# Kernel tuning notes

Hardware: AMD Instinct MI355X
Metric: run time of the kernel (lower is better)

The kernel has to match this reference:

```python
import jax, jax.numpy as jnp
import numpy as np

IMG_H, IMG_W = 240, 320
NEAR, FAR = 0.1, 10.0
CHUNK = 64  # triangles rasterized per scan step
CAM_K = np.array([[286.2057, 0.0, 162.6306],
                  [0.0, 286.7852, 121.0245],
                  [0.0, 0.0, 1.0]], np.float32)


def build_projection(cam, w, h, x0=0, y0=0, nc=NEAR, fc=FAR):
    q = -(fc + nc) / float(fc - nc)
    qn = -2.0 * fc * nc / float(fc - nc)
    proj = np.array([
        [2 * cam[0, 0] / w, -2 * cam[0, 1] / w, (-2 * cam[0, 2] + w + 2 * x0) / w, 0],
        [0, -2 * cam[1, 1] / h, (-2 * cam[1, 2] + h + 2 * y0) / h, 0],
        [0, 0, q, qn],
        [0, 0, -1, 0]], dtype=np.float64)
    proj[1, :] *= -1.0
    return jnp.asarray(proj.T, jnp.float32)


def vertex_normals(verts, faces):
    # per-face normal scattered to its vertices then renormalized
    # (equals dirt lighting.vertex_normals_pre_split on split meshes)
    v0, v1, v2 = verts[faces[:, 0]], verts[faces[:, 1]], verts[faces[:, 2]]
    fn = jnp.cross(v1 - v0, v2 - v0)
    fn = fn / jnp.maximum(jnp.linalg.norm(fn, axis=1, keepdims=True), 1e-12)
    vn = (jnp.zeros_like(verts)
          .at[faces[:, 0]].add(fn)
          .at[faces[:, 1]].add(fn)
          .at[faces[:, 2]].add(fn))
    return vn / jnp.maximum(jnp.linalg.norm(vn, axis=1, keepdims=True), 1e-12)


def transform_vertices(vertices, pose, faces, proj):
    vert_obj = jnp.concatenate([vertices, jnp.ones_like(vertices[:, -1:])], axis=1)  # [V,4]
    normals = vertex_normals(vert_obj[:, :3], faces)
    gl = jnp.array([[1., 0., 0.], [0., -1., 0.], [0., 0., -1.]], jnp.float32)
    rot = gl @ pose[:3, :3]
    # replicate the flat-list surgery: cam_pose[:3,:3]=gl@R, negate t_y, t_z
    cam_pose = pose.at[:3, :3].set(rot).at[1, 3].multiply(-1.0).at[2, 3].multiply(-1.0)
    view = cam_pose.T
    vert_cam = vert_obj @ view                                   # [V,4]
    vert_3d = vert_obj[:, :3] @ pose[:3, :3].T + pose[:3, 3]     # [V,3]
    vert_clip = vert_cam @ proj                                  # [V,4]
    return vert_obj, vert_3d, vert_clip, normals


def rasterise(vert_clip, colors, faces, H, W):
    # z-buffered triangle rasterization with perspective-correct barycentric
    # interpolation, processed in chunks of CHUNK triangles via lax.scan.
    eps = 1e-9
    wc = vert_clip[:, 3]
    inv_w = 1.0 / jnp.where(jnp.abs(wc) > eps, wc, eps)
    ndc = vert_clip[:, :3] * inv_w[:, None]
    px = (ndc[:, 0] + 1.0) * 0.5 * W   # screen x
    py = (1.0 - ndc[:, 1]) * 0.5 * H   # screen y (row 0 at top)
    pz = ndc[:, 2]

    tpx, tpy, tpz = px[faces], py[faces], pz[faces]   # [F,3]
    tiw = inv_w[faces]                                # [F,3]
    tcol = colors[faces]                              # [F,3,C]
    tval = jnp.all(wc[faces] > 1e-6, axis=1)          # all verts in front

    F = faces.shape[0]
    pad = (-F) % CHUNK
    def padf(a):
        if pad == 0:
            return a
        return jnp.concatenate([a, jnp.zeros((pad,) + a.shape[1:], a.dtype)], 0)
    tpx, tpy, tpz, tiw, tcol = padf(tpx), padf(tpy), padf(tpz), padf(tiw), padf(tcol)
    tval = padf(tval)
    n_steps = (F + pad) // CHUNK
    resh = lambda a: a.reshape((n_steps, CHUNK) + a.shape[1:])
    xs = tuple(map(resh, (tpx, tpy, tpz, tiw, tcol, tval)))

    Xg = (jnp.arange(W, dtype=jnp.float32) + 0.5)[None, :, None]  # pixel centers
    Yg = (jnp.arange(H, dtype=jnp.float32) + 0.5)[:, None, None]
    BIG = jnp.float32(1e9)

    def step(carry, chunk):
        zbuf, cbuf = carry
        cpx, cpy, cpz, ciw, ccol, cval = chunk
        ax, ay = cpx[:, 0], cpy[:, 0]
        bx, by = cpx[:, 1], cpy[:, 1]
        cx, cy = cpx[:, 2], cpy[:, 2]
        area = (bx - ax) * (cy - ay) - (by - ay) * (cx - ax)            # [Fc]
        inv_area = 1.0 / jnp.where(jnp.abs(area) > 1e-12, area, 1e-12)
        # normalized edge functions (barycentrics), [H,W,Fc]
        e0 = ((Xg - bx) * (cy - by) - (Yg - by) * (cx - bx)) * inv_area
        e1 = ((Xg - cx) * (ay - cy) - (Yg - cy) * (ax - cx)) * inv_area
        e2 = 1.0 - e0 - e1
        depth = e0 * cpz[:, 0] + e1 * cpz[:, 1] + e2 * cpz[:, 2]        # screen-linear z
        inside = ((e0 >= 0) & (e1 >= 0) & (e2 >= 0) & cval
                  & (jnp.abs(area) > 1e-12) & (depth >= -1.0) & (depth <= 1.0))
        dmask = jnp.where(inside, depth, BIG)
        best = jnp.argmin(dmask, axis=2)                                # [H,W]
        bidx = best[..., None]
        bdepth = jnp.take_along_axis(dmask, bidx, 2)[..., 0]
        take = bdepth < zbuf
        b0 = jnp.take_along_axis(e0, bidx, 2)[..., 0]
        b1 = jnp.take_along_axis(e1, bidx, 2)[..., 0]
        b2 = 1.0 - b0 - b1
        piw = jnp.stack([b0, b1, b2], -1) * ciw[best]                   # [H,W,3]
        den = jnp.sum(piw, -1, keepdims=True)
        den = jnp.where(jnp.abs(den) > 1e-12, den, 1e-12)
        col = jnp.einsum('hwk,hwkc->hwc', piw / den, ccol[best])        # persp-correct
        zbuf = jnp.where(take, bdepth, zbuf)
        cbuf = jnp.where(take[..., None], col, cbuf)
        return (zbuf, cbuf), None

    zbuf0 = jnp.full((H, W), BIG, jnp.float32)
    cbuf0 = jnp.zeros((H, W, colors.shape[1]), jnp.float32)
    (_, cbuf), _ = jax.lax.scan(jax.checkpoint(step), (zbuf0, cbuf0), xs)
    return cbuf


def setup_inputs() -> dict:
    key = jax.random.key(0)
    k1, k2 = jax.random.split(key)
    V, F = 12288, 4096
    vertices = 0.15 * jax.random.normal(k1, (1, V, 3), jnp.float32)
    faces = jax.random.randint(k2, (1, F, 3), 0, V, jnp.int32)
    pose = jnp.eye(4, dtype=jnp.float32).at[2, 3].set(0.6)  # object 0.6m in front
    return {"vertices": vertices, "faces": faces, "poses": pose[None]}


def reference(vertices, faces, poses):
    proj = build_projection(CAM_K, IMG_W, IMG_H)
    faces0 = jnp.asarray(faces[0], jnp.int32)
    vert_obj, vert_3d, vert_clip, normals = transform_vertices(vertices[0], poses[0], faces0, proj)
    colors = jnp.concatenate(
        [jnp.ones_like(vert_obj[:, :1]), vert_3d, normals, vert_obj], axis=1)  # [V,11]
    g = rasterise(vert_clip, colors, faces0, IMG_H, IMG_W)  # [H,W,11]
    return g[None]
```

## Files before the change

### kernel.cpp

```cpp
#include <hip/hip_runtime.h>
#include <math.h>

#pragma clang fp contract(off)

#define IMG_H 240
#define IMG_W 320
#define NPX   (IMG_H * IMG_W)
#define NCH   11
#define NCHP  12
#define NSLICE 8
#define CULL_M 1e-3f
#define EZ_M   1e-5f

struct ProjM { float m[16]; };

extern "C" __global__ void k_init(float* __restrict__ vnacc, int n3v,
                                  unsigned long long* __restrict__ zkey) {
  int i = blockIdx.x * 256 + threadIdx.x;
  if (i < n3v) vnacc[i] = 0.0f;
  if (i < NPX) zkey[i] = ~0ull;
}

__device__ __forceinline__ void xform(float x, float y, float z,
                                      const float* __restrict__ pose,
                                      const ProjM& P,
                                      float& px, float& py, float& pz,
                                      float& iw, float& wc) {
  float c0 = ((x*pose[0]     + y*pose[1])     + z*pose[2])     + pose[3];
  float c1 = ((x*(-pose[4])  + y*(-pose[5]))  + z*(-pose[6]))  + (-pose[7]);
  float c2 = ((x*(-pose[8])  + y*(-pose[9]))  + z*(-pose[10])) + (-pose[11]);
  float c3 = ((x*pose[12]    + y*pose[13])    + z*pose[14])    + pose[15];
  float q0 = ((c0*P.m[0]  + c1*P.m[1])  + c2*P.m[2])  + c3*P.m[3];
  float q1 = ((c0*P.m[4]  + c1*P.m[5])  + c2*P.m[6])  + c3*P.m[7];
  float q2 = ((c0*P.m[8]  + c1*P.m[9])  + c2*P.m[10]) + c3*P.m[11];
  float q3 = ((c0*P.m[12] + c1*P.m[13]) + c2*P.m[14]) + c3*P.m[15];
  wc = q3;
  float denw = (fabsf(wc) > 1e-9f) ? wc : 1e-9f;
  iw = 1.0f / denw;
  float ndx = q0 * iw, ndy = q1 * iw;
  pz = q2 * iw;
  px = ((ndx + 1.0f) * 0.5f) * (float)IMG_W;
  py = ((1.0f - ndy) * 0.5f) * (float)IMG_H;
}

extern "C" __global__ void k_face(const float* __restrict__ verts,
                                  const int* __restrict__ faces,
                                  const float* __restrict__ pose,
                                  ProjM P,
                                  float* __restrict__ vnacc,
                                  float4* __restrict__ frec,
                                  float4* __restrict__ fbb,
                                  float4* __restrict__ fe,
                                  int4*  __restrict__ fidx, int F) {
  int f = blockIdx.x * 64 + threadIdx.x;
  if (f >= F) return;
  int i0 = faces[3*f+0], i1 = faces[3*f+1], i2 = faces[3*f+2];
  float x0 = verts[3*i0+0], y0 = verts[3*i0+1], z0 = verts[3*i0+2];
  float x1 = verts[3*i1+0], y1 = verts[3*i1+1], z1 = verts[3*i1+2];
  float x2 = verts[3*i2+0], y2 = verts[3*i2+1], z2 = verts[3*i2+2];

  {
    float ux = x1 - x0, uy = y1 - y0, uz = z1 - z0;
    float vx = x2 - x0, vy = y2 - y0, vz = z2 - z0;
    float fx = uy*vz - uz*vy;
    float fy = uz*vx - ux*vz;
    float fz = ux*vy - uy*vx;
    float n = sqrtf((fx*fx + fy*fy) + fz*fz);
    float d = fmaxf(n, 1e-12f);
    fx = fx / d; fy = fy / d; fz = fz / d;
    atomicAdd(&vnacc[3*i0+0], fx); atomicAdd(&vnacc[3*i0+1], fy); atomicAdd(&vnacc[3*i0+2], fz);
    atomicAdd(&vnacc[3*i1+0], fx); atomicAdd(&vnacc[3*i1+1], fy); atomicAdd(&vnacc[3*i1+2], fz);
    atomicAdd(&vnacc[3*i2+0], fx); atomicAdd(&vnacc[3*i2+1], fy); atomicAdd(&vnacc[3*i2+2], fz);
  }

  float ax, ay, pz0, iw0, w0;  xform(x0, y0, z0, pose, P, ax, ay, pz0, iw0, w0);
  float bx, by, pz1, iw1, w1;  xform(x1, y1, z1, pose, P, bx, by, pz1, iw1, w1);
  float cx, cy, pz2, iw2, w2;  xform(x2, y2, z2, pose, P, cx, cy, pz2, iw2, w2);

  float area = (bx - ax) * (cy - ay) - (by - ay) * (cx - ax);
  float inva = 1.0f / ((fabsf(area) > 1e-12f) ? area : 1e-12f);
  bool valid = (w0 > 1e-6f) && (w1 > 1e-6f) && (w2 > 1e-6f) && (fabsf(area) > 1e-12f);
  float rax = 2.0f*cx - ax, ray = 2.0f*cy - ay;
  float rbx = 2.0f*cx - bx, rby = 2.0f*cy - by;
  float minx = fminf(cx, fminf(rax, rbx)), maxx = fmaxf(cx, fmaxf(rax, rbx));
  float miny = fminf(cy, fminf(ray, rby)), maxy = fmaxf(cy, fmaxf(ray, rby));
  frec[4*f+0] = make_float4(bx, by, cy - by, cx - bx);
  frec[4*f+1] = make_float4(cx, cy, ay - cy, ax - cx);
  frec[4*f+2] = make_float4(inva, pz0, pz1, pz2);
  frec[4*f+3] = make_float4(iw0, iw1, iw2, 0.0f);
  fbb[f] = valid ? make_float4(minx, maxx, miny, maxy)
                 : make_float4(1e30f, -1e30f, 1e30f, -1e30f);
  fidx[f] = make_int4(i0, i1, i2, 0);
  {
    double dbx = bx, dby = by, dcx = cx, dcy = cy, dax = ax, day = ay;
    double dinv = (double)inva;
    double d0 = dcy - dby, d1 = dcx - dbx;
    double d2 = day - dcy, d3 = dax - dcx;
    double a0 = d0 * dinv, b0 = -d1 * dinv, c0 = (dby * d1 - dbx * d0) * dinv;
    double a1 = d2 * dinv, b1 = -d3 * dinv, c1 = (dcy * d3 - dcx * d2) * dinv;
    fe[2*f+0] = make_float4((float)a0, (float)b0, (float)c0, 0.0f);
    fe[2*f+1] = make_float4((float)a1, (float)b1, (float)c1, 0.0f);
  }
}

extern "C" __global__ void k_vertex(const float* __restrict__ verts,
                                    const float* __restrict__ vnacc,
                                    const float* __restrict__ pose,
                                    float4* __restrict__ colors, int V) {
  int i = blockIdx.x * 64 + threadIdx.x;
  if (i >= V) return;
  float x = verts[3*i+0], y = verts[3*i+1], z = verts[3*i+2];

  float nx = vnacc[3*i+0], ny = vnacc[3*i+1], nz = vnacc[3*i+2];
  float nn = sqrtf((nx*nx + ny*ny) + nz*nz);
  float nm = fmaxf(nn, 1e-12f);
  nx = nx / nm; ny = ny / nm; nz = nz / nm;

  float v3x = ((x*pose[0] + y*pose[1]) + z*pose[2])  + pose[3];
  float v3y = ((x*pose[4] + y*pose[5]) + z*pose[6])  + pose[7];
  float v3z = ((x*pose[8] + y*pose[9]) + z*pose[10]) + pose[11];

  colors[3*i+0] = make_float4(1.0f, v3x, v3y, v3z);
  colors[3*i+1] = make_float4(nx, ny, nz, x);
  colors[3*i+2] = make_float4(y, z, 1.0f, 0.0f);
}

extern "C" __global__ __launch_bounds__(256)
void k_rasterA(const float4* __restrict__ frec,
               const float4* __restrict__ fbb,
               const float4* __restrict__ fe,
               unsigned long long* __restrict__ zkey,
               int F, int nslice) {
  int t = threadIdx.x;
  int wave = t >> 6;
  int lane = t & 63;
  int sx = (wave & 1) * 8, sy = (wave >> 1) * 8;
  int pxi = blockIdx.x * 16 + sx + (lane & 7);
  int pyi = blockIdx.y * 16 + sy + (lane >> 3);
  float X = (float)pxi + 0.5f;
  float Y = (float)pyi + 0.5f;
  float tXlo = (float)(blockIdx.x * 16 + sx) + 0.5f, tXhi = tXlo + 7.0f;
  float tYlo = (float)(blockIdx.y * 16 + sy) + 0.5f, tYhi = tYlo + 7.0f;

  int f0 = blockIdx.z * nslice;
  int f1 = min(F, f0 + nslice);

  float bestd = 1e9f;
  int   besti = -1;

  for (int base = f0; base < f1; base += 64) {
    int f = base + lane;
    bool ov = false;
    if (f < f1) {
      float4 bb = fbb[f];
      ov = (bb.x - 1.0f <= tXhi) && (bb.y + 1.0f >= tXlo) &&
           (bb.z - 1.0f <= tYhi) && (bb.w + 1.0f >= tYlo);
      if (ov) {
        float4 E0 = fe[2*f+0];
        float4 E1 = fe[2*f+1];
        float pa0 = E0.x * tXlo, pb0 = E0.x * tXhi;
        float qa0 = E0.y * tYlo, qb0 = E0.y * tYhi;
        float e0mx = (fmaxf(pa0, pb0) + fmaxf(qa0, qb0)) + E0.z;
        float e0mn = (fminf(pa0, pb0) + fminf(qa0, qb0)) + E0.z;
        float pa1 = E1.x * tXlo, pb1 = E1.x * tXhi;
        float qa1 = E1.y * tYlo, qb1 = E1.y * tYhi;
        float e1mx = (fmaxf(pa1, pb1) + fmaxf(qa1, qb1)) + E1.z;
        float e1mn = (fminf(pa1, pb1) + fminf(qa1, qb1)) + E1.z;
        float e2mx = (1.0f - e0mn) - e1mn;
        ov = (e0mx >= -CULL_M) && (e1mx >= -CULL_M) && (e2mx >= -CULL_M);
      }
    }
    unsigned long long mask = __ballot(ov);

    while (mask) {
      int j = __builtin_ctzll(mask);
      mask &= mask - 1;
      int ju = __builtin_amdgcn_readfirstlane(base + j);
      const float4* fr = frec + (size_t)ju * 4;
      float4 C = fr[2];
      float zminf = fminf(C.y, fminf(C.z, C.w));
      if (__ballot(bestd > zminf - EZ_M) == 0ull) continue;
      float4 A = fr[0];
      float4 B = fr[1];
      float t0 = (X - A.x) * A.z;
      float t1 = (Y - A.y) * A.w;
      float e0 = (t0 - t1) * C.x;
      float t2 = (X - B.x) * B.z;
      float t3 = (Y - B.y) * B.w;
      float e1 = (t2 - t3) * C.x;
      float e2 = (1.0f - e0) - e1;
      float depth = ((e0 * C.y) + (e1 * C.z)) + (e2 * C.w);
      bool inside = (e0 >= 0.0f) && (e1 >= 0.0f) && (e2 >= 0.0f) &&
                    (depth >= -1.0f) && (depth <= 1.0f);
      if (inside && depth < bestd) {
        bestd = depth; besti = base + j;
      }
    }
  }

  if (besti >= 0) {
    unsigned int ub = __float_as_uint(bestd);
    ub = (ub & 0x80000000u) ? ~ub : (ub | 0x80000000u);
    unsigned long long key = ((unsigned long long)ub << 32) | (unsigned int)besti;
    atomicMin(&zkey[(size_t)pyi * IMG_W + pxi], key);
  }
}

extern "C" __global__ __launch_bounds__(256)
void k_resolve(const unsigned long long* __restrict__ zkey,
               const float4* __restrict__ frec,
               const float4* __restrict__ colors,
               const int4* __restrict__ fidx,
               float* __restrict__ out) {
  __shared__ float sOut[256 * NCH];
  int t = threadIdx.x;
  int p = blockIdx.x * 256 + t;
  int pyi = p / IMG_W, pxi = p - pyi * IMG_W;
  float X = (float)pxi + 0.5f;
  float Y = (float)pyi + 0.5f;
  unsigned long long key = zkey[p];

  float oc[NCH];
  if (key != ~0ull) {
    int besti = (int)(key & 0xFFFFFFFFu);
    const float4* fr = frec + (size_t)besti * 4;
    float4 A = fr[0], B = fr[1], C = fr[2], D = fr[3];
    float t0 = (X - A.x) * A.z;
    float t1 = (Y - A.y) * A.w;
    float e0 = (t0 - t1) * C.x;
    float t2 = (X - B.x) * B.z;
    float t3 = (Y - B.y) * B.w;
    float e1 = (t2 - t3) * C.x;
    float b2 = (1.0f - e0) - e1;
    float p0 = e0 * D.x, p1 = e1 * D.y, p2 = b2 * D.z;
    float den = (p0 + p1) + p2;
    if (!(fabsf(den) > 1e-12f)) den = 1e-12f;
    float u0 = p0 / den, u1 = p1 / den, u2 = p2 / den;
    int4 vi = fidx[besti];
    float c0v[NCHP], c1v[NCHP], c2v[NCHP];
    #pragma unroll
    for (int k = 0; k < 3; ++k) {
      *(float4*)(c0v + 4*k) = colors[3*vi.x + k];
      *(float4*)(c1v + 4*k) = colors[3*vi.y + k];
      *(float4*)(c2v + 4*k) = colors[3*vi.z + k];
    }
    #pragma unroll
    for (int ch = 0; ch < NCH; ++ch)
      oc[ch] = (u0 * c0v[ch] + u1 * c1v[ch]) + u2 * c2v[ch];
  } else {
    #pragma unroll
    for (int ch = 0; ch < NCH; ++ch) oc[ch] = 0.0f;
  }
  #pragma unroll
  for (int ch = 0; ch < NCH; ++ch) sOut[t * NCH + ch] = oc[ch];
  __syncthreads();
  float4* o4 = (float4*)(out + (size_t)blockIdx.x * 256 * NCH);
  const float4* s4 = (const float4*)sOut;
  #pragma unroll
  for (int k = 0; k < 3; ++k) {
    int idx = t + k * 256;
    if (idx < 704) o4[idx] = s4[idx];
  }
}

extern "C" void kernel_launch(void* const* d_in, const int* in_sizes, int n_in,
                              void* d_out, int out_size, void* d_ws, size_t ws_size,
                              hipStream_t stream) {
  const float* verts = (const float*)d_in[0];
  const int*   faces = (const int*)d_in[1];
  const float* pose  = (const float*)d_in[2];
  float* out = (float*)d_out;
  int V = in_sizes[0] / 3;
  int F = in_sizes[1] / 3;

  float* ws = (float*)d_ws;
  size_t o = 0;
  auto alloc = [&](size_t n) { size_t r = o; o += (n + 3) & ~(size_t)3; return r; };
  size_t o_zk   = alloc((size_t)2 * NPX);
  size_t o_vn   = alloc((size_t)3 * V);
  size_t o_col  = alloc((size_t)NCHP * V);
  size_t o_fr   = alloc((size_t)16 * F);
  size_t o_bb   = alloc((size_t)4 * F);
  size_t o_fe   = alloc((size_t)8 * F);
  size_t o_fi   = alloc((size_t)4 * F);
  unsigned long long* zkey = (unsigned long long*)(ws + o_zk);
  float*  vnacc = ws + o_vn;
  float4* col   = (float4*)(ws + o_col);
  float4* frec  = (float4*)(ws + o_fr);
  float4* fbb   = (float4*)(ws + o_bb);
  float4* fe    = (float4*)(ws + o_fe);
  int4*   fidx  = (int4*)(ws + o_fi);

  double fxd = 286.2057, sd = 0.0, cxd = 162.6306;
  double fyd = 286.7852, cyd = 121.0245;
  double wd = IMG_W, hd = IMG_H, ncd = 0.1, fcd = 10.0;
  double q  = -(fcd + ncd) / (fcd - ncd);
  double qn = -2.0 * fcd * ncd / (fcd - ncd);
  double Pd[16] = {
    2.0*fxd/wd, -2.0*sd/wd, (-2.0*cxd + wd)/wd, 0.0,
    0.0,        2.0*fyd/hd, (2.0*cyd - hd)/hd, -0.0,
    0.0,        0.0,        q,                  qn,
    0.0,        0.0,       -1.0,                0.0 };
  ProjM P;
  for (int i = 0; i < 16; ++i) P.m[i] = (float)Pd[i];

  int n3v = 3 * V;
  int initN = (NPX > n3v) ? NPX : n3v;
  k_init<<<(initN + 255) / 256, 256, 0, stream>>>(vnacc, n3v, zkey);
  k_face<<<(F + 63) / 64, 64, 0, stream>>>(verts, faces, pose, P, vnacc,
                                           frec, fbb, fe, fidx, F);
  k_vertex<<<(V + 63) / 64, 64, 0, stream>>>(verts, vnacc, pose, col, V);
  int nslice = (F + NSLICE - 1) / NSLICE;
  dim3 g(IMG_W / 16, IMG_H / 16, NSLICE);
  k_rasterA<<<g, 256, 0, stream>>>(frec, fbb, fe, zkey, F, nslice);
  k_resolve<<<NPX / 256, 256, 0, stream>>>(zkey, frec, col, fidx, out);
}
```

Measured before the change: 91.02 us.

## Depth-sort faces into buckets and early-exit rasterization per tile, fusing resolve

Adds a single-block bucket sort of faces by minimum depth, plus per-chunk suffix minima of depth. A fused per-8x8-tile raster kernel walks faces front-to-back and stops once no lane can improve its depth. This removes the face-slice split, the global 64-bit atomicMin z-buffer, the init kernel and the separate resolve pass, and it writes output directly from the raster kernel. In exchange it adds a serial one-block sort launch and gives each tile a single wave with no slice parallelism, which may hurt occupancy when the early exit prunes little.

```diff
diff --git a/kernel.cpp b/kernel.cpp
--- a/kernel.cpp
+++ b/kernel.cpp
@@ -8,18 +8,12 @@
 #define NPX   (IMG_H * IMG_W)
 #define NCH   11
 #define NCHP  12
-#define NSLICE 8
+#define MAXF  4096
+#define NBUCK 1024
 #define CULL_M 1e-3f
 #define EZ_M   1e-5f
 
 struct ProjM { float m[16]; };
-
-extern "C" __global__ void k_init(float* __restrict__ vnacc, int n3v,
-                                  unsigned long long* __restrict__ zkey) {
-  int i = blockIdx.x * 256 + threadIdx.x;
-  if (i < n3v) vnacc[i] = 0.0f;
-  if (i < NPX) zkey[i] = ~0ull;
-}
 
 __device__ __forceinline__ void xform(float x, float y, float z,
                                       const float* __restrict__ pose,
@@ -51,8 +45,9 @@
                                   float4* __restrict__ frec,
                                   float4* __restrict__ fbb,
                                   float4* __restrict__ fe,
-                                  int4*  __restrict__ fidx, int F) {
-  int f = blockIdx.x * 64 + threadIdx.x;
+                                  int4*  __restrict__ fidx,
+                                  float* __restrict__ zmin, int F) {
+  int f = blockIdx.x * 256 + threadIdx.x;
   if (f >= F) return;
   int i0 = faces[3*f+0], i1 = faces[3*f+1], i2 = faces[3*f+2];
   float x0 = verts[3*i0+0], y0 = verts[3*i0+1], z0 = verts[3*i0+2];
@@ -91,6 +86,7 @@
   fbb[f] = valid ? make_float4(minx, maxx, miny, maxy)
                  : make_float4(1e30f, -1e30f, 1e30f, -1e30f);
   fidx[f] = make_int4(i0, i1, i2, 0);
+  zmin[f] = valid ? fminf(pz0, fminf(pz1, pz2)) : 3.0e38f;
   {
     double dbx = bx, dby = by, dcx = cx, dcy = cy, dax = ax, day = ay;
     double dinv = (double)inva;
@@ -103,11 +99,101 @@
   }
 }
 
+extern "C" __global__ __launch_bounds__(1024)
+void k_sort(const float* __restrict__ zmin,
+            int* __restrict__ perm,
+            float* __restrict__ chunkz, int F) {
+  __shared__ unsigned int hist[NBUCK];
+  __shared__ unsigned int scanA[NBUCK];
+  __shared__ float zs[MAXF];
+  __shared__ float redmin[16], redmax[16];
+  __shared__ float zloS, scaleS;
+  __shared__ float cm[64];
+  int t = threadIdx.x;
+  int lane = t & 63, wid = t >> 6;
+
+  float zv[4]; int ff[4];
+  float lmin = 3.0e38f, lmax = -3.0e38f;
+  #pragma unroll
+  for (int k = 0; k < 4; ++k) {
+    int f = t + k * 1024;
+    ff[k] = f;
+    float z = (f < F) ? zmin[f] : 3.0e38f;
+    zv[k] = z;
+    if (z < 1.0e37f) { lmin = fminf(lmin, z); lmax = fmaxf(lmax, z); }
+  }
+  #pragma unroll
+  for (int off = 32; off > 0; off >>= 1) {
+    lmin = fminf(lmin, __shfl_down(lmin, off));
+    lmax = fmaxf(lmax, __shfl_down(lmax, off));
+  }
+  if (lane == 0) { redmin[wid] = lmin; redmax[wid] = lmax; }
+  for (int i = t; i < NBUCK; i += 1024) hist[i] = 0;
+  __syncthreads();
+  if (t == 0) {
+    float zlo = 3.0e38f, zhi = -3.0e38f;
+    for (int i = 0; i < 16; ++i) {
+      zlo = fminf(zlo, redmin[i]); zhi = fmaxf(zhi, redmax[i]);
+    }
+    zloS = zlo;
+    scaleS = (zhi > zlo) ? ((float)(NBUCK - 1) / (zhi - zlo)) : 0.0f;
+  }
+  __syncthreads();
+  float zlo = zloS, scale = scaleS;
+
+  unsigned bk[4];
+  #pragma unroll
+  for (int k = 0; k < 4; ++k) {
+    float b = fminf((float)(NBUCK - 1), fmaxf(0.0f, (zv[k] - zlo) * scale));
+    bk[k] = (unsigned)b;
+    if (ff[k] < F) atomicAdd(&hist[bk[k]], 1u);
+  }
+  __syncthreads();
+
+  unsigned cnt = hist[t];
+  scanA[t] = cnt;
+  __syncthreads();
+  for (int d = 1; d < NBUCK; d <<= 1) {
+    unsigned add = (t >= d) ? scanA[t - d] : 0u;
+    __syncthreads();
+    scanA[t] += add;
+    __syncthreads();
+  }
+  hist[t] = scanA[t] - cnt;
+  __syncthreads();
+
+  #pragma unroll
+  for (int k = 0; k < 4; ++k) {
+    if (ff[k] < F) {
+      unsigned pos = atomicAdd(&hist[bk[k]], 1u);
+      perm[pos] = ff[k];
+      zs[pos] = zv[k];
+    }
+  }
+  __syncthreads();
+
+  int nch = (F + 63) >> 6;
+  if (t < nch) {
+    float m = 3.0e38f;
+    for (int i = 0; i < 64; ++i) {
+      int p = t * 64 + i;
+      if (p < F) m = fminf(m, zs[p]);
+    }
+    cm[t] = m;
+  }
+  __syncthreads();
+  if (t < nch) {
+    float s = 3.0e38f;
+    for (int c = t; c < nch; ++c) s = fminf(s, cm[c]);
+    chunkz[t] = s;
+  }
+}
+
 extern "C" __global__ void k_vertex(const float* __restrict__ verts,
                                     const float* __restrict__ vnacc,
                                     const float* __restrict__ pose,
                                     float4* __restrict__ colors, int V) {
-  int i = blockIdx.x * 64 + threadIdx.x;
+  int i = blockIdx.x * 256 + threadIdx.x;
   if (i >= V) return;
   float x = verts[3*i+0], y = verts[3*i+1], z = verts[3*i+2];
 
@@ -125,33 +211,36 @@
   colors[3*i+2] = make_float4(y, z, 1.0f, 0.0f);
 }
 
-extern "C" __global__ __launch_bounds__(256)
-void k_rasterA(const float4* __restrict__ frec,
-               const float4* __restrict__ fbb,
-               const float4* __restrict__ fe,
-               unsigned long long* __restrict__ zkey,
-               int F, int nslice) {
-  int t = threadIdx.x;
-  int wave = t >> 6;
-  int lane = t & 63;
-  int sx = (wave & 1) * 8, sy = (wave >> 1) * 8;
-  int pxi = blockIdx.x * 16 + sx + (lane & 7);
-  int pyi = blockIdx.y * 16 + sy + (lane >> 3);
+extern "C" __global__ __launch_bounds__(64)
+void k_raster(const float4* __restrict__ frec,
+              const float4* __restrict__ fbb,
+              const float4* __restrict__ fe,
+              const int* __restrict__ perm,
+              const float* __restrict__ chunkz,
+              const float4* __restrict__ colors,
+              const int4* __restrict__ fidx,
+              float* __restrict__ out, int F) {
+  __shared__ float sOut[64 * NCH];
+  int lane = threadIdx.x;
+  int px0 = blockIdx.x * 8, py0 = blockIdx.y * 8;
+  int pxi = px0 + (lane & 7), pyi = py0 + (lane >> 3);
   float X = (float)pxi + 0.5f;
   float Y = (float)pyi + 0.5f;
-  float tXlo = (float)(blockIdx.x * 16 + sx) + 0.5f, tXhi = tXlo + 7.0f;
-  float tYlo = (float)(blockIdx.y * 16 + sy) + 0.5f, tYhi = tYlo + 7.0f;
-
-  int f0 = blockIdx.z * nslice;
-  int f1 = min(F, f0 + nslice);
-
+  float tXlo = (float)px0 + 0.5f, tXhi = tXlo + 7.0f;
+  float tYlo = (float)py0 + 0.5f, tYhi = tYlo + 7.0f;
+
+  unsigned long long bestkey = ~0ull;
   float bestd = 1e9f;
-  int   besti = -1;
-
-  for (int base = f0; base < f1; base += 64) {
-    int f = base + lane;
+
+  int nch = (F + 63) >> 6;
+  for (int c = 0; c < nch; ++c) {
+    if (__ballot(bestd > chunkz[c] - EZ_M) == 0ull) break;
+
+    int idx = c * 64 + lane;
+    int f = 0;
     bool ov = false;
-    if (f < f1) {
+    if (idx < F) {
+      f = perm[idx];
       float4 bb = fbb[f];
       ov = (bb.x - 1.0f <= tXhi) && (bb.y + 1.0f >= tXlo) &&
            (bb.z - 1.0f <= tYhi) && (bb.w + 1.0f >= tYlo);
@@ -175,8 +264,8 @@
     while (mask) {
       int j = __builtin_ctzll(mask);
       mask &= mask - 1;
-      int ju = __builtin_amdgcn_readfirstlane(base + j);
-      const float4* fr = frec + (size_t)ju * 4;
+      int fid = __shfl(f, j);
+      const float4* fr = frec + (size_t)fid * 4;
       float4 C = fr[2];
       float zminf = fminf(C.y, fminf(C.z, C.w));
       if (__ballot(bestd > zminf - EZ_M) == 0ull) continue;
@@ -192,37 +281,18 @@
       float depth = ((e0 * C.y) + (e1 * C.z)) + (e2 * C.w);
       bool inside = (e0 >= 0.0f) && (e1 >= 0.0f) && (e2 >= 0.0f) &&
                     (depth >= -1.0f) && (depth <= 1.0f);
-      if (inside && depth < bestd) {
-        bestd = depth; besti = base + j;
+      if (inside) {
+        unsigned int ub = __float_as_uint(depth);
+        ub = (ub & 0x80000000u) ? ~ub : (ub | 0x80000000u);
+        unsigned long long key = ((unsigned long long)ub << 32) | (unsigned int)fid;
+        if (key < bestkey) { bestkey = key; bestd = depth; }
       }
     }
   }
 
-  if (besti >= 0) {
-    unsigned int ub = __float_as_uint(bestd);
-    ub = (ub & 0x80000000u) ? ~ub : (ub | 0x80000000u);
-    unsigned long long key = ((unsigned long long)ub << 32) | (unsigned int)besti;
-    atomicMin(&zkey[(size_t)pyi * IMG_W + pxi], key);
-  }
-}
-
-extern "C" __global__ __launch_bounds__(256)
-void k_resolve(const unsigned long long* __restrict__ zkey,
-               const float4* __restrict__ frec,
-               const float4* __restrict__ colors,
-               const int4* __restrict__ fidx,
-               float* __restrict__ out) {
-  __shared__ float sOut[256 * NCH];
-  int t = threadIdx.x;
-  int p = blockIdx.x * 256 + t;
-  int pyi = p / IMG_W, pxi = p - pyi * IMG_W;
-  float X = (float)pxi + 0.5f;
-  float Y = (float)pyi + 0.5f;
-  unsigned long long key = zkey[p];
-
   float oc[NCH];
-  if (key != ~0ull) {
-    int besti = (int)(key & 0xFFFFFFFFu);
+  if (bestkey != ~0ull) {
+    int besti = (int)(bestkey & 0xFFFFFFFFu);
     const float4* fr = frec + (size_t)besti * 4;
     float4 A = fr[0], B = fr[1], C = fr[2], D = fr[3];
     float t0 = (X - A.x) * A.z;
@@ -252,14 +322,13 @@
     for (int ch = 0; ch < NCH; ++ch) oc[ch] = 0.0f;
   }
   #pragma unroll
-  for (int ch = 0; ch < NCH; ++ch) sOut[t * NCH + ch] = oc[ch];
-  __syncthreads();
-  float4* o4 = (float4*)(out + (size_t)blockIdx.x * 256 * NCH);
+  for (int ch = 0; ch < NCH; ++ch) sOut[lane * NCH + ch] = oc[ch];
+  __syncthreads();
   const float4* s4 = (const float4*)sOut;
-  #pragma unroll
-  for (int k = 0; k < 3; ++k) {
-    int idx = t + k * 256;
-    if (idx < 704) o4[idx] = s4[idx];
+  for (int i = lane; i < 176; i += 64) {
+    int r = i / 22, cc = i - r * 22;
+    float4* go = (float4*)(out + ((size_t)(py0 + r) * IMG_W + px0) * NCH);
+    go[cc] = s4[r * 22 + cc];
   }
 }
 
@@ -276,20 +345,24 @@
   float* ws = (float*)d_ws;
   size_t o = 0;
   auto alloc = [&](size_t n) { size_t r = o; o += (n + 3) & ~(size_t)3; return r; };
-  size_t o_zk   = alloc((size_t)2 * NPX);
   size_t o_vn   = alloc((size_t)3 * V);
   size_t o_col  = alloc((size_t)NCHP * V);
   size_t o_fr   = alloc((size_t)16 * F);
   size_t o_bb   = alloc((size_t)4 * F);
   size_t o_fe   = alloc((size_t)8 * F);
   size_t o_fi   = alloc((size_t)4 * F);
-  unsigned long long* zkey = (unsigned long long*)(ws + o_zk);
+  size_t o_zm   = alloc((size_t)F);
+  size_t o_pm   = alloc((size_t)F);
+  size_t o_cz   = alloc((size_t)64);
   float*  vnacc = ws + o_vn;
   float4* col   = (float4*)(ws + o_col);
   float4* frec  = (float4*)(ws + o_fr);
   float4* fbb   = (float4*)(ws + o_bb);
   float4* fe    = (float4*)(ws + o_fe);
   int4*   fidx  = (int4*)(ws + o_fi);
+  float*  zmin  = ws + o_zm;
+  int*    perm  = (int*)(ws + o_pm);
+  float*  chz   = ws + o_cz;
 
   double fxd = 286.2057, sd = 0.0, cxd = 162.6306;
   double fyd = 286.7852, cyd = 121.0245;
@@ -304,14 +377,11 @@
   ProjM P;
   for (int i = 0; i < 16; ++i) P.m[i] = (float)Pd[i];
 
-  int n3v = 3 * V;
-  int initN = (NPX > n3v) ? NPX : n3v;
-  k_init<<<(initN + 255) / 256, 256, 0, stream>>>(vnacc, n3v, zkey);
-  k_face<<<(F + 63) / 64, 64, 0, stream>>>(verts, faces, pose, P, vnacc,
-                                           frec, fbb, fe, fidx, F);
-  k_vertex<<<(V + 63) / 64, 64, 0, stream>>>(verts, vnacc, pose, col, V);
-  int nslice = (F + NSLICE - 1) / NSLICE;
-  dim3 g(IMG_W / 16, IMG_H / 16, NSLICE);
-  k_rasterA<<<g, 256, 0, stream>>>(frec, fbb, fe, zkey, F, nslice);
-  k_resolve<<<NPX / 256, 256, 0, stream>>>(zkey, frec, col, fidx, out);
-}
+  hipMemsetAsync(vnacc, 0, (size_t)3 * V * sizeof(float), stream);
+  k_face<<<(F + 255) / 256, 256, 0, stream>>>(verts, faces, pose, P, vnacc,
+                                              frec, fbb, fe, fidx, zmin, F);
+  k_sort<<<1, 1024, 0, stream>>>(zmin, perm, chz, F);
+  k_vertex<<<(V + 255) / 256, 256, 0, stream>>>(verts, vnacc, pose, col, V);
+  dim3 g(IMG_W / 8, IMG_H / 8);
+  k_raster<<<g, 64, 0, stream>>>(frec, fbb, fe, perm, chz, col, fidx, out, F);
+}
```

Result: slower. 122.2 us (+34.2%).
